# Optimization experiments

Hardware: AMD Instinct MI355X
Metric: run time of the kernel (lower is better)

Reference implementation:

```python
import jax, jax.numpy as jnp
import numpy as np

N_NODES = 50000
N_EDGES = 600000
N_GRAPHS = 256
N_FL1, N_MPL, N_FL2, N_FL3 = 128, 128, 128, 64
EPS = 1e-12


def _glorot(key, shape):
    lim = float(np.sqrt(6.0 / (shape[0] + shape[1])))
    return jax.random.uniform(key, shape, jnp.float32, -lim, lim)


def setup_inputs() -> dict:
    key = jax.random.key(0)
    ks = jax.random.split(key, 16)
    x = jax.random.normal(ks[0], (N_NODES, 5), jnp.float32)
    edge_index = jax.random.randint(ks[1], (2, N_EDGES), 0, N_NODES, jnp.int64)
    batch = jnp.sort(jax.random.randint(ks[2], (N_NODES,), 0, N_GRAPHS, jnp.int64))
    return {
        "x": x,
        "edge_index": edge_index,
        "batch": batch,
        "W_pre": _glorot(ks[3], (5, N_FL1)),
        "b_pre": jnp.zeros((N_FL1,), jnp.float32),
        "W1_l": _glorot(ks[4], (N_FL1, N_MPL)),
        "b1": jnp.zeros((N_MPL,), jnp.float32),
        "W1_r": _glorot(ks[5], (N_FL1, N_MPL)),
        "W2_l": _glorot(ks[6], (N_MPL, N_MPL)),
        "b2": jnp.zeros((N_MPL,), jnp.float32),
        "W2_r": _glorot(ks[7], (N_MPL, N_MPL)),
        "W_p1": _glorot(ks[8], (N_MPL, N_FL2)),
        "b_p1": jnp.zeros((N_FL2,), jnp.float32),
        "W_p2": _glorot(ks[9], (N_FL2, N_FL3)),
        "b_p2": jnp.zeros((N_FL3,), jnp.float32),
        "W_out": _glorot(ks[10], (N_FL3, 1)),
        "b_out": jnp.zeros((1,), jnp.float32),
    }


def _sage_conv(x, src, dst, deg_inv, W_l, b_l, W_r):
    # mean-aggregate neighbor messages x[src] onto dst, then linear transforms
    agg = jax.ops.segment_sum(x[src], dst, num_segments=N_NODES) * deg_inv  # [N, d]
    out = agg @ W_l + b_l + x @ W_r
    # normalize=True -> L2 normalize per node (PyG F.normalize, eps=1e-12)
    norm = jnp.sqrt(jnp.sum(out * out, axis=-1, keepdims=True))
    return out / jnp.maximum(norm, EPS)


def reference(x, edge_index, batch, W_pre, b_pre, W1_l, b1, W1_r,
              W2_l, b2, W2_r, W_p1, b_p1, W_p2, b_p2, W_out, b_out):
    src, dst = edge_index[0], edge_index[1]
    deg = jax.ops.segment_sum(jnp.ones((N_EDGES,), jnp.float32), dst, num_segments=N_NODES)
    deg_inv = (1.0 / jnp.maximum(deg, 1.0))[:, None]

    h = jax.nn.relu(x @ W_pre + b_pre)
    h = jax.nn.relu(_sage_conv(h, src, dst, deg_inv, W1_l, b1, W1_r))
    h = jax.nn.relu(_sage_conv(h, src, dst, deg_inv, W2_l, b2, W2_r))

    # global_mean_pool over graph ids in batch
    g_sum = jax.ops.segment_sum(h, batch, num_segments=N_GRAPHS)  # [G, d]
    g_cnt = jax.ops.segment_sum(jnp.ones((N_NODES,), jnp.float32), batch, num_segments=N_GRAPHS)
    g = g_sum / jnp.maximum(g_cnt, 1.0)[:, None]

    g = jax.nn.relu(g @ W_p1 + b_p1)
    g = jax.nn.relu(g @ W_p2 + b_p2)
    return g @ W_out + b_out  # [G, 1]
```

## Files before the change

kernel.cpp:

```cpp
#include <hip/hip_runtime.h>
#include <hip/hip_bf16.h>

#define N_NODES 50000
#define N_EDGES 600000
#define N_GRAPHS 256
#define D 128
#define NTILES 1563

typedef __bf16 bf16x8 __attribute__((ext_vector_type(8)));
typedef float f32x16 __attribute__((ext_vector_type(16)));
typedef unsigned short u16x8 __attribute__((ext_vector_type(8)));

__device__ __forceinline__ float bf2f(unsigned short u) {
    unsigned v = ((unsigned)u) << 16;
    return __builtin_bit_cast(float, v);
}
__device__ __forceinline__ unsigned short f2bf(float f) {
    unsigned x = __builtin_bit_cast(unsigned, f);
    unsigned r = (x + 0x7fffu + ((x >> 16) & 1u)) >> 16;
    return (unsigned short)r;
}


__global__ void zero_int_kernel(int* __restrict__ p, int n) {
    int i = blockIdx.x * 256 + threadIdx.x;
    if (i < n) p[i] = 0;
}

__global__ void deg_kernel(const int* __restrict__ dst, int* __restrict__ deg) {
    int e = blockIdx.x * 256 + threadIdx.x;
    if (e < N_EDGES) atomicAdd(&deg[dst[e]], 1);
}

__global__ __launch_bounds__(1024) void scan_blk_kernel(const int* __restrict__ deg,
                                                        int* __restrict__ partial,
                                                        int* __restrict__ bsum) {
    __shared__ int tmp[1024];
    int tid = threadIdx.x;
    int i = blockIdx.x * 1024 + tid;
    int v = (i < N_NODES) ? deg[i] : 0;
    tmp[tid] = v;
    __syncthreads();
    for (int off = 1; off < 1024; off <<= 1) {
        int add = (tid >= off) ? tmp[tid - off] : 0;
        __syncthreads();
        tmp[tid] += add;
        __syncthreads();
    }
    if (i < N_NODES) partial[i] = tmp[tid] - v;
    if (tid == 1023) bsum[blockIdx.x] = tmp[tid];
}

__global__ void scan_top_kernel(const int* __restrict__ bsum, int* __restrict__ boff,
                                int* __restrict__ row_start, int nblk) {
    int l = threadIdx.x;
    int v = (l < nblk) ? bsum[l] : 0;
    int incl = v;
#pragma unroll
    for (int m = 1; m < 64; m <<= 1) {
        int t = __shfl_up(incl, m);
        if (l >= m) incl += t;
    }
    if (l < nblk) boff[l] = incl - v;
    if (l == 63) row_start[N_NODES] = incl;
}

__global__ void scan_fix_kernel(const int* __restrict__ partial, const int* __restrict__ boff,
                                const int* __restrict__ deg, int* __restrict__ row_start,
                                int* __restrict__ cursor, float* __restrict__ deg_inv) {
    int i = blockIdx.x * 256 + threadIdx.x;
    if (i >= N_NODES) return;
    int rs = partial[i] + boff[i >> 10];
    row_start[i] = rs;
    cursor[i] = rs;
    deg_inv[i] = 1.0f / fmaxf((float)deg[i], 1.0f);
}

__global__ void fill_kernel(const int* __restrict__ src, const int* __restrict__ dst,
                            int* __restrict__ cursor, int* __restrict__ csr_src) {
    int e = blockIdx.x * 256 + threadIdx.x;
    if (e < N_EDGES) {
        int slot = atomicAdd(&cursor[dst[e]], 1);
        csr_src[slot] = src[e];
    }
}


__global__ void pack_w_kernel(const float* __restrict__ Wl1, const float* __restrict__ Wr1,
                              const float* __restrict__ Wl2, const float* __restrict__ Wr2,
                              unsigned short* __restrict__ Wp) {
    int tid = blockIdx.x * 256 + threadIdx.x;
    int conv = tid >> 15;
    int e = tid & 32767;
    int j = e & 7, lane = (e >> 3) & 63, ct = (e >> 9) & 3, kt = e >> 11;
    int k = kt * 16 + (lane >> 5) * 8 + j;
    int col = ct * 32 + (lane & 31);
    const float* Wl = conv ? Wl2 : Wl1;
    const float* Wr = conv ? Wr2 : Wr1;
    float v = (k < 128) ? Wl[k * 128 + col] : Wr[(k - 128) * 128 + col];
    Wp[tid] = f2bf(v);
}


__global__ void pre_kernel(const float* __restrict__ x, const float* __restrict__ Wp,
                           const float* __restrict__ bp, unsigned short* __restrict__ h0) {
    int idx = blockIdx.x * 256 + threadIdx.x;
    if (idx >= N_NODES * 32) return;
    int node = idx >> 5, j4 = (idx & 31) * 4;
    const float* xr = x + node * 5;
    float4 acc = *(const float4*)&bp[j4];
#pragma unroll
    for (int k = 0; k < 5; ++k) {
        float xv = xr[k];
        float4 w = *(const float4*)&Wp[k * D + j4];
        acc.x += xv * w.x; acc.y += xv * w.y; acc.z += xv * w.z; acc.w += xv * w.w;
    }
    ushort4 o;
    o.x = f2bf(fmaxf(acc.x, 0.f));
    o.y = f2bf(fmaxf(acc.y, 0.f));
    o.z = f2bf(fmaxf(acc.z, 0.f));
    o.w = f2bf(fmaxf(acc.w, 0.f));
    *(ushort4*)&h0[(size_t)node * D + j4] = o;
}


__global__ __launch_bounds__(256) void agg_kernel(const unsigned short* __restrict__ h,
                                                  const int* __restrict__ row_start,
                                                  const int* __restrict__ csr_src,
                                                  const float* __restrict__ deg_inv,
                                                  unsigned short* __restrict__ aggb) {
    int node = blockIdx.x * 4 + (threadIdx.x >> 6);
    int lane = threadIdx.x & 63;
    if (node >= N_NODES) return;
    int grp = lane >> 4;
    int fl = lane & 15;
    int s = row_start[node], e = row_start[node + 1];
    float a[8] = {0.f, 0.f, 0.f, 0.f, 0.f, 0.f, 0.f, 0.f};
    int i = s + grp;
    for (; i + 4 < e; i += 8) {
        int c0 = csr_src[i];
        int c1 = csr_src[i + 4];
        bf16x8 v0 = *(const bf16x8*)(h + (size_t)c0 * D + fl * 8);
        bf16x8 v1 = *(const bf16x8*)(h + (size_t)c1 * D + fl * 8);
#pragma unroll
        for (int j = 0; j < 8; ++j) a[j] += (float)v0[j] + (float)v1[j];
    }
    if (i < e) {
        int c0 = csr_src[i];
        bf16x8 v0 = *(const bf16x8*)(h + (size_t)c0 * D + fl * 8);
#pragma unroll
        for (int j = 0; j < 8; ++j) a[j] += (float)v0[j];
    }
#pragma unroll
    for (int j = 0; j < 8; ++j) {
        a[j] += __shfl_xor(a[j], 16);
        a[j] += __shfl_xor(a[j], 32);
    }
    if (grp == 0) {
        float di = deg_inv[node];
        u16x8 o;
#pragma unroll
        for (int j = 0; j < 8; ++j) o[j] = f2bf(a[j] * di);
        *(u16x8*)(aggb + (size_t)node * D + fl * 8) = o;
    }
}


__global__ __launch_bounds__(256) void lin_mfma_kernel(const unsigned short* __restrict__ hin,
                                                       const unsigned short* __restrict__ aggb,
                                                       const unsigned short* __restrict__ Wp,
                                                       const float* __restrict__ b,
                                                       unsigned short* __restrict__ hout) {
    int wg = blockIdx.x * 4 + (threadIdx.x >> 6);
    if (wg >= NTILES) return;
    int lane = threadIdx.x & 63;
    int l31 = lane & 31, hi = lane >> 5;
    int row0 = wg * 32;
    int rowg = row0 + l31;
    if (rowg > N_NODES - 1) rowg = N_NODES - 1;

    const unsigned short* arow = aggb + (size_t)rowg * D + hi * 8;
    const unsigned short* hrow = hin + (size_t)rowg * D + hi * 8;
    const unsigned short* wbase = Wp + lane * 8;

    f32x16 acc[4];
#pragma unroll
    for (int ct = 0; ct < 4; ++ct) acc[ct] = (f32x16)(0.0f);

#pragma unroll
    for (int kt = 0; kt < 16; ++kt) {
        const unsigned short* asrc = (kt < 8) ? (arow + kt * 16) : (hrow + (kt - 8) * 16);
        bf16x8 af = *(const bf16x8*)asrc;
#pragma unroll
        for (int ct = 0; ct < 4; ++ct) {
            bf16x8 bfrag = *(const bf16x8*)(wbase + (kt * 4 + ct) * 512);
            acc[ct] = __builtin_amdgcn_mfma_f32_32x32x16_bf16(af, bfrag, acc[ct], 0, 0, 0);
        }
    }

    float bb[4];
#pragma unroll
    for (int ct = 0; ct < 4; ++ct) bb[ct] = b[ct * 32 + l31];

#pragma unroll
    for (int r = 0; r < 16; ++r) {
        float v0 = acc[0][r] + bb[0];
        float v1 = acc[1][r] + bb[1];
        float v2 = acc[2][r] + bb[2];
        float v3 = acc[3][r] + bb[3];
        float ss = v0 * v0 + v1 * v1 + v2 * v2 + v3 * v3;
        ss += __shfl_xor(ss, 1);
        ss += __shfl_xor(ss, 2);
        ss += __shfl_xor(ss, 4);
        ss += __shfl_xor(ss, 8);
        ss += __shfl_xor(ss, 16);
        float sc = 1.0f / fmaxf(sqrtf(ss), 1e-12f);
        int row = row0 + (r & 3) + 8 * (r >> 2) + 4 * hi;
        if (row < N_NODES) {
            size_t o = (size_t)row * D + l31;
            hout[o] = f2bf(fmaxf(v0 * sc, 0.f));
            hout[o + 32] = f2bf(fmaxf(v1 * sc, 0.f));
            hout[o + 64] = f2bf(fmaxf(v2 * sc, 0.f));
            hout[o + 96] = f2bf(fmaxf(v3 * sc, 0.f));
        }
    }
}


__global__ __launch_bounds__(128) void pool_sum_kernel(const unsigned short* __restrict__ h,
                                                       const int* __restrict__ batch,
                                                       float* __restrict__ gsum) {
    int j = threadIdx.x;
    int i0 = blockIdx.x * 128;
    int i1 = i0 + 128;
    if (i1 > N_NODES) i1 = N_NODES;
    __shared__ int bids[128];
    if (i0 + j < N_NODES) bids[j] = batch[i0 + j];
    __syncthreads();
    float acc = 0.f;
    int cur = bids[0];
    for (int i = i0; i < i1; ++i) {
        int bid = bids[i - i0];
        if (bid != cur) {
            atomicAdd(&gsum[cur * D + j], acc);
            acc = 0.f;
            cur = bid;
        }
        acc += bf2f(h[(size_t)i * D + j]);
    }
    atomicAdd(&gsum[cur * D + j], acc);
}


__global__ __launch_bounds__(128) void mlp_kernel(const float* __restrict__ gsum,
                                                  const int* __restrict__ batch,
                                                  const float* __restrict__ Wp1,
                                                  const float* __restrict__ bp1,
                                                  const float* __restrict__ Wp2,
                                                  const float* __restrict__ bp2,
                                                  const float* __restrict__ Wout,
                                                  const float* __restrict__ bout,
                                                  float* __restrict__ out) {
    __shared__ float gin[128], y1[128], y2[64];
    __shared__ float cnt_s;
    int gid = blockIdx.x, j = threadIdx.x;
    if (j == 0) {
        int lo = 0, hi = N_NODES;
        while (lo < hi) { int m = (lo + hi) >> 1; if (batch[m] < gid) lo = m + 1; else hi = m; }
        int start = lo;
        lo = start; hi = N_NODES;
        while (lo < hi) { int m = (lo + hi) >> 1; if (batch[m] < gid + 1) lo = m + 1; else hi = m; }
        cnt_s = fmaxf((float)(lo - start), 1.0f);
    }
    __syncthreads();
    gin[j] = gsum[gid * 128 + j] / cnt_s;
    __syncthreads();
    float a = bp1[j];
    for (int k = 0; k < 128; ++k) a += gin[k] * Wp1[k * 128 + j];
    y1[j] = fmaxf(a, 0.f);
    __syncthreads();
    if (j < 64) {
        float a2 = bp2[j];
        for (int k = 0; k < 128; ++k) a2 += y1[k] * Wp2[k * 64 + j];
        y2[j] = fmaxf(a2, 0.f);
    }
    __syncthreads();
    if (j < 64) {
        float v = y2[j] * Wout[j];
#pragma unroll
        for (int m = 32; m >= 1; m >>= 1) v += __shfl_xor(v, m);
        if (j == 0) out[gid] = v + bout[0];
    }
}


extern "C" void kernel_launch(void* const* d_in, const int* in_sizes, int n_in,
                              void* d_out, int out_size, void* d_ws, size_t ws_size,
                              hipStream_t stream) {
    const float* x     = (const float*)d_in[0];
    const int*   ei    = (const int*)d_in[1];
    const int*   batch = (const int*)d_in[2];
    const float* W_pre = (const float*)d_in[3];
    const float* b_pre = (const float*)d_in[4];
    const float* W1_l  = (const float*)d_in[5];
    const float* b1    = (const float*)d_in[6];
    const float* W1_r  = (const float*)d_in[7];
    const float* W2_l  = (const float*)d_in[8];
    const float* b2    = (const float*)d_in[9];
    const float* W2_r  = (const float*)d_in[10];
    const float* W_p1  = (const float*)d_in[11];
    const float* b_p1  = (const float*)d_in[12];
    const float* W_p2  = (const float*)d_in[13];
    const float* b_p2  = (const float*)d_in[14];
    const float* W_out = (const float*)d_in[15];
    const float* b_out = (const float*)d_in[16];

    const int* src = ei;
    const int* dst = ei + N_EDGES;

    size_t off = 0;
    auto carve = [&](size_t bytes) {
        void* p = (char*)d_ws + off;
        off += (bytes + 255) & ~(size_t)255;
        return p;
    };
    int* deg       = (int*)carve(50048 * 4 + 32768 * 4);
    float* gsum    = (float*)(deg + 50048);
    int* row_start = (int*)carve((N_NODES + 1) * 4);
    int* cursor    = (int*)carve(N_NODES * 4);
    int* csr_src   = (int*)carve(N_EDGES * 4);
    float* deg_inv = (float*)carve(N_NODES * 4);
    int* partial   = (int*)carve(N_NODES * 4);
    int* bsum      = (int*)carve(64 * 4);
    int* boff      = (int*)carve(64 * 4);
    unsigned short* h0   = (unsigned short*)carve((size_t)N_NODES * D * 2);
    unsigned short* h1   = (unsigned short*)carve((size_t)N_NODES * D * 2);
    unsigned short* aggb = (unsigned short*)carve((size_t)N_NODES * D * 2);
    unsigned short* Wp   = (unsigned short*)carve(65536 * 2);
    unsigned short* h2 = h0;
    float* out = (float*)d_out;

    const int nblk_scan = (N_NODES + 1023) / 1024;

    pack_w_kernel<<<256, 256, 0, stream>>>(W1_l, W1_r, W2_l, W2_r, Wp);

    zero_int_kernel<<<(50048 + 32768 + 255) / 256, 256, 0, stream>>>(deg, 50048 + 32768);
    deg_kernel<<<(N_EDGES + 255) / 256, 256, 0, stream>>>(dst, deg);
    scan_blk_kernel<<<nblk_scan, 1024, 0, stream>>>(deg, partial, bsum);
    scan_top_kernel<<<1, 64, 0, stream>>>(bsum, boff, row_start, nblk_scan);
    scan_fix_kernel<<<(N_NODES + 255) / 256, 256, 0, stream>>>(partial, boff, deg,
                                                               row_start, cursor, deg_inv);
    fill_kernel<<<(N_EDGES + 255) / 256, 256, 0, stream>>>(src, dst, cursor, csr_src);

    pre_kernel<<<(N_NODES * 32 + 255) / 256, 256, 0, stream>>>(x, W_pre, b_pre, h0);

    agg_kernel<<<(N_NODES + 3) / 4, 256, 0, stream>>>(h0, row_start, csr_src, deg_inv, aggb);
    lin_mfma_kernel<<<(NTILES + 3) / 4, 256, 0, stream>>>(h0, aggb, Wp, b1, h1);

    agg_kernel<<<(N_NODES + 3) / 4, 256, 0, stream>>>(h1, row_start, csr_src, deg_inv, aggb);
    lin_mfma_kernel<<<(NTILES + 3) / 4, 256, 0, stream>>>(h1, aggb, Wp + 32768, b2, h2);

    pool_sum_kernel<<<(N_NODES + 127) / 128, 128, 0, stream>>>(h2, batch, gsum);
    mlp_kernel<<<N_GRAPHS, 128, 0, stream>>>(gsum, batch, W_p1, b_p1, W_p2, b_p2,
                                             W_out, b_out, out);
}
```

Before: 225.5 us.

## Use one 16-lane group per node in aggregation and interleave weight columns for vector stores

The aggregation kernel now gives each node a 16-lane group that walks all its neighbors with a 4-way unrolled loop, where before a full wavefront split the neighbors across four groups and combined them with shuffles. This removes the cross-group shuffle reduction and the idle lanes on low-degree nodes, at the cost of a longer serial loop per node. The packed weights are permuted so each lane owns four adjacent output columns, which turns the four scattered 2-byte stores in the linear kernel into one 8-byte store. The pre-transform kernel also writes 8 features per thread.

```diff
diff --git a/kernel.cpp b/kernel.cpp
--- a/kernel.cpp
+++ b/kernel.cpp
@@ -10,6 +10,7 @@
 typedef __bf16 bf16x8 __attribute__((ext_vector_type(8)));
 typedef float f32x16 __attribute__((ext_vector_type(16)));
 typedef unsigned short u16x8 __attribute__((ext_vector_type(8)));
+typedef unsigned short u16x4 __attribute__((ext_vector_type(4)));
 
 __device__ __forceinline__ float bf2f(unsigned short u) {
     unsigned v = ((unsigned)u) << 16;
@@ -94,7 +95,7 @@
     int e = tid & 32767;
     int j = e & 7, lane = (e >> 3) & 63, ct = (e >> 9) & 3, kt = e >> 11;
     int k = kt * 16 + (lane >> 5) * 8 + j;
-    int col = ct * 32 + (lane & 31);
+    int col = (lane & 31) * 4 + ct;
     const float* Wl = conv ? Wl2 : Wl1;
     const float* Wr = conv ? Wr2 : Wr1;
     float v = (k < 128) ? Wl[k * 128 + col] : Wr[(k - 128) * 128 + col];
@@ -105,22 +106,22 @@
 __global__ void pre_kernel(const float* __restrict__ x, const float* __restrict__ Wp,
                            const float* __restrict__ bp, unsigned short* __restrict__ h0) {
     int idx = blockIdx.x * 256 + threadIdx.x;
-    if (idx >= N_NODES * 32) return;
-    int node = idx >> 5, j4 = (idx & 31) * 4;
+    if (idx >= N_NODES * 16) return;
+    int node = idx >> 4, j8 = (idx & 15) * 8;
     const float* xr = x + node * 5;
-    float4 acc = *(const float4*)&bp[j4];
+    float acc[8];
+#pragma unroll
+    for (int c = 0; c < 8; ++c) acc[c] = bp[j8 + c];
 #pragma unroll
     for (int k = 0; k < 5; ++k) {
         float xv = xr[k];
-        float4 w = *(const float4*)&Wp[k * D + j4];
-        acc.x += xv * w.x; acc.y += xv * w.y; acc.z += xv * w.z; acc.w += xv * w.w;
-    }
-    ushort4 o;
-    o.x = f2bf(fmaxf(acc.x, 0.f));
-    o.y = f2bf(fmaxf(acc.y, 0.f));
-    o.z = f2bf(fmaxf(acc.z, 0.f));
-    o.w = f2bf(fmaxf(acc.w, 0.f));
-    *(ushort4*)&h0[(size_t)node * D + j4] = o;
+#pragma unroll
+        for (int c = 0; c < 8; ++c) acc[c] += xv * Wp[k * D + j8 + c];
+    }
+    u16x8 o;
+#pragma unroll
+    for (int c = 0; c < 8; ++c) o[c] = f2bf(fmaxf(acc[c], 0.f));
+    *(u16x8*)&h0[(size_t)node * D + j8] = o;
 }
 
 
@@ -129,40 +130,36 @@
                                                   const int* __restrict__ csr_src,
                                                   const float* __restrict__ deg_inv,
                                                   unsigned short* __restrict__ aggb) {
-    int node = blockIdx.x * 4 + (threadIdx.x >> 6);
-    int lane = threadIdx.x & 63;
+    int node = blockIdx.x * 16 + (threadIdx.x >> 4);
+    int fl = threadIdx.x & 15;
     if (node >= N_NODES) return;
-    int grp = lane >> 4;
-    int fl = lane & 15;
     int s = row_start[node], e = row_start[node + 1];
     float a[8] = {0.f, 0.f, 0.f, 0.f, 0.f, 0.f, 0.f, 0.f};
-    int i = s + grp;
-    for (; i + 4 < e; i += 8) {
+    int i = s;
+    for (; i + 3 < e; i += 4) {
         int c0 = csr_src[i];
-        int c1 = csr_src[i + 4];
+        int c1 = csr_src[i + 1];
+        int c2 = csr_src[i + 2];
+        int c3 = csr_src[i + 3];
         bf16x8 v0 = *(const bf16x8*)(h + (size_t)c0 * D + fl * 8);
         bf16x8 v1 = *(const bf16x8*)(h + (size_t)c1 * D + fl * 8);
-#pragma unroll
-        for (int j = 0; j < 8; ++j) a[j] += (float)v0[j] + (float)v1[j];
-    }
-    if (i < e) {
+        bf16x8 v2 = *(const bf16x8*)(h + (size_t)c2 * D + fl * 8);
+        bf16x8 v3 = *(const bf16x8*)(h + (size_t)c3 * D + fl * 8);
+#pragma unroll
+        for (int j = 0; j < 8; ++j)
+            a[j] += ((float)v0[j] + (float)v1[j]) + ((float)v2[j] + (float)v3[j]);
+    }
+    for (; i < e; ++i) {
         int c0 = csr_src[i];
         bf16x8 v0 = *(const bf16x8*)(h + (size_t)c0 * D + fl * 8);
 #pragma unroll
         for (int j = 0; j < 8; ++j) a[j] += (float)v0[j];
     }
-#pragma unroll
-    for (int j = 0; j < 8; ++j) {
-        a[j] += __shfl_xor(a[j], 16);
-        a[j] += __shfl_xor(a[j], 32);
-    }
-    if (grp == 0) {
-        float di = deg_inv[node];
-        u16x8 o;
-#pragma unroll
-        for (int j = 0; j < 8; ++j) o[j] = f2bf(a[j] * di);
-        *(u16x8*)(aggb + (size_t)node * D + fl * 8) = o;
-    }
+    float di = deg_inv[node];
+    u16x8 o;
+#pragma unroll
+    for (int j = 0; j < 8; ++j) o[j] = f2bf(a[j] * di);
+    *(u16x8*)(aggb + (size_t)node * D + fl * 8) = o;
 }
 
 
@@ -198,17 +195,18 @@
         }
     }
 
-    float bb[4];
-#pragma unroll
-    for (int ct = 0; ct < 4; ++ct) bb[ct] = b[ct * 32 + l31];
+    float4 b4 = *(const float4*)&b[l31 * 4];
+    float bb[4] = {b4.x, b4.y, b4.z, b4.w};
 
 #pragma unroll
     for (int r = 0; r < 16; ++r) {
-        float v0 = acc[0][r] + bb[0];
-        float v1 = acc[1][r] + bb[1];
-        float v2 = acc[2][r] + bb[2];
-        float v3 = acc[3][r] + bb[3];
-        float ss = v0 * v0 + v1 * v1 + v2 * v2 + v3 * v3;
+        float v[4];
+        float ss = 0.f;
+#pragma unroll
+        for (int ct = 0; ct < 4; ++ct) {
+            v[ct] = acc[ct][r] + bb[ct];
+            ss += v[ct] * v[ct];
+        }
         ss += __shfl_xor(ss, 1);
         ss += __shfl_xor(ss, 2);
         ss += __shfl_xor(ss, 4);
@@ -217,11 +215,10 @@
         float sc = 1.0f / fmaxf(sqrtf(ss), 1e-12f);
         int row = row0 + (r & 3) + 8 * (r >> 2) + 4 * hi;
         if (row < N_NODES) {
-            size_t o = (size_t)row * D + l31;
-            hout[o] = f2bf(fmaxf(v0 * sc, 0.f));
-            hout[o + 32] = f2bf(fmaxf(v1 * sc, 0.f));
-            hout[o + 64] = f2bf(fmaxf(v2 * sc, 0.f));
-            hout[o + 96] = f2bf(fmaxf(v3 * sc, 0.f));
+            u16x4 o;
+#pragma unroll
+            for (int ct = 0; ct < 4; ++ct) o[ct] = f2bf(fmaxf(v[ct] * sc, 0.f));
+            *(u16x4*)(hout + (size_t)row * D + l31 * 4) = o;
         }
     }
 }
@@ -352,12 +349,12 @@
                                                                row_start, cursor, deg_inv);
     fill_kernel<<<(N_EDGES + 255) / 256, 256, 0, stream>>>(src, dst, cursor, csr_src);
 
-    pre_kernel<<<(N_NODES * 32 + 255) / 256, 256, 0, stream>>>(x, W_pre, b_pre, h0);
-
-    agg_kernel<<<(N_NODES + 3) / 4, 256, 0, stream>>>(h0, row_start, csr_src, deg_inv, aggb);
+    pre_kernel<<<(N_NODES * 16 + 255) / 256, 256, 0, stream>>>(x, W_pre, b_pre, h0);
+
+    agg_kernel<<<(N_NODES + 15) / 16, 256, 0, stream>>>(h0, row_start, csr_src, deg_inv, aggb);
     lin_mfma_kernel<<<(NTILES + 3) / 4, 256, 0, stream>>>(h0, aggb, Wp, b1, h1);
 
-    agg_kernel<<<(N_NODES + 3) / 4, 256, 0, stream>>>(h1, row_start, csr_src, deg_inv, aggb);
+    agg_kernel<<<(N_NODES + 15) / 16, 256, 0, stream>>>(h1, row_start, csr_src, deg_inv, aggb);
     lin_mfma_kernel<<<(NTILES + 3) / 4, 256, 0, stream>>>(h1, aggb, Wp + 32768, b2, h2);
 
     pool_sum_kernel<<<(N_NODES + 127) / 128, 128, 0, stream>>>(h2, batch, gsum);
```

New measurement: 215.3 us. 1.05x faster.
